# Performance work log

Measured on AMD Instinct MI355X. Metric: run time of the kernel, lower is better.

The kernel has to match this reference:

```python
import jax, jax.numpy as jnp
import numpy as np
from jax import lax


def setup_inputs() -> dict:
    key = jax.random.key(0)
    ks = jax.random.split(key, 8)
    B, H, W = 1, 128, 128

    def rnd(k, shape, fan_in):
        return jax.random.normal(k, shape, dtype=jnp.float32) / np.float32(np.sqrt(fan_in))

    return {
        "x": jax.random.normal(ks[0], (B, 1, H, W), dtype=jnp.float32),
        "z": jax.random.uniform(ks[1], (B, 1), dtype=jnp.float32),
        "w_conv1": rnd(ks[2], (16, 1, 9, 9), 81),
        "b_conv1": jnp.zeros((16,), jnp.float32),
        "w_conv2": rnd(ks[3], (16, 16, 5, 5), 16 * 25),
        "b_conv2": jnp.zeros((16,), jnp.float32),
        "w_fc1": rnd(ks[4], (1024, 128), 1024),
        "b_fc1": jnp.zeros((128,), jnp.float32),
        "w_pose": rnd(ks[5], (1, 16), 1),
        "b_pose": jnp.zeros((16,), jnp.float32),
        "w_fc2": rnd(ks[6], (144, 1), 144),
        "b_fc2": jnp.zeros((1,), jnp.float32),
    }


_DN = ("NCHW", "OIHW", "NCHW")  # conv dimension numbers
_P = 32  # GQ-CNN patch size


def _maxpool2(h):
    return lax.reduce_window(h, -jnp.inf, lax.max, (1, 1, 2, 2), (1, 1, 2, 2), "VALID")


def _gqcnn(patches, z_rep, w_conv1, b_conv1, w_conv2, b_conv2,
           w_fc1, b_fc1, w_pose, b_pose, w_fc2, b_fc2):
    # patches: [N,1,32,32], z_rep: [N,1] -> quality [N,1]
    h = jax.nn.relu(lax.conv_general_dilated(patches, w_conv1, (1, 1), "SAME",
                                             dimension_numbers=_DN)
                    + b_conv1[None, :, None, None])
    h = _maxpool2(h)  # [N,16,16,16]
    h = jax.nn.relu(lax.conv_general_dilated(h, w_conv2, (1, 1), "SAME",
                                             dimension_numbers=_DN)
                    + b_conv2[None, :, None, None])
    h = _maxpool2(h)  # [N,16,8,8]
    flat = h.reshape(h.shape[0], -1)  # [N,1024]
    f = jax.nn.relu(flat @ w_fc1 + b_fc1)      # [N,128]
    p = jax.nn.relu(z_rep @ w_pose + b_pose)   # [N,16]
    return jnp.concatenate([f, p], axis=1) @ w_fc2 + b_fc2  # [N,1]


def reference(x, z, w_conv1, b_conv1, w_conv2, b_conv2,
              w_fc1, b_fc1, w_pose, b_pose, w_fc2, b_fc2):
    B, _, H, W = x.shape
    Hp, Wp = H - _P, W - _P  # loop ranges in the original: range(H-32), range(W-32)
    # Batched patch extraction replaces the O(H*W) Python loop.
    pat = lax.conv_general_dilated_patches(x, (_P, _P), (1, 1), "VALID")  # [B,1024,H-31,W-31]
    pat = pat[:, :, :Hp, :Wp]
    pat = jnp.transpose(pat, (0, 2, 3, 1)).reshape(B * Hp * Wp, 1, _P, _P)
    z_rep = jnp.repeat(z, Hp * Wp, axis=0)  # matches [B,Hp,Wp] flattening order
    q = _gqcnn(pat, z_rep, w_conv1, b_conv1, w_conv2, b_conv2,
               w_fc1, b_fc1, w_pose, b_pose, w_fc2, b_fc2)  # [N,1]
    half = _P // 2
    heat = jnp.zeros_like(x).at[:, :, half:H - half, half:W - half].set(
        q.reshape(B, 1, Hp, Wp))
    return heat
```

## Files before the change

### kernel.cpp

```cpp
#include <hip/hip_runtime.h>

typedef __attribute__((ext_vector_type(8))) short short8;
typedef __attribute__((ext_vector_type(4))) float f32x4;
typedef unsigned short u16;

__device__ __forceinline__ u16 f2bf(float f) {
    unsigned u = __builtin_bit_cast(unsigned, f);
    unsigned r = u + 0x7fffu + ((u >> 16) & 1u);
    return (u16)(r >> 16);
}
__device__ __forceinline__ unsigned pkbf(float lo, float hi) {
    unsigned r;
    asm("v_cvt_pk_bf16_f32 %0, %1, %2" : "=v"(r) : "v"(lo), "v"(hi));
    return r;
}

__global__ __launch_bounds__(256) void k0_prep(
    const float* __restrict__ z, const float* __restrict__ w1,
    const float* __restrict__ w2, const float* __restrict__ wfc1,
    const float* __restrict__ wpose, const float* __restrict__ bpose,
    const float* __restrict__ wfc2, const float* __restrict__ bfc2,
    float* __restrict__ out, u16* __restrict__ w1p, u16* __restrict__ w2p,
    u16* __restrict__ fc1T, float* __restrict__ cst)
{
    int gt = blockIdx.x * 256 + threadIdx.x;
    out[gt] = 0.f;

    if (gt < 2560) {
        int l = (gt >> 3) & 63, j = gt & 7, s = gt >> 9;
        int o = l & 15, bq = l >> 4;
        u16 v = 0;
        if (bq < 3) {
            int dx = bq * 4 + (j & 3);
            int dy = -1;
            if (s < 4) dy = 2 * s + (j >> 2);
            else if (j < 4) dy = 8;
            if (dy >= 0 && dx <= 8) v = f2bf(w1[o * 81 + dy * 9 + dx]);
        }
        w1p[gt] = v;
    }
    if (gt < 6656) {
        int l = (gt >> 3) & 63, j = gt & 7, s = gt >> 9;
        int o = l & 15, bq = l >> 4;
        int dy, dx, c8; bool valid = true;
        if (s < 5)       { dy = s;     dx = bq >> 1;       c8 = bq & 1; }
        else if (s < 10) { dy = s - 5; dx = 2 + (bq >> 1); c8 = bq & 1; }
        else { dy = (s - 10) + 3 * (bq & 1); dx = 4; c8 = bq >> 1; valid = (dy <= 4); }
        int ci = c8 * 8 + j;
        w2p[gt] = valid ? f2bf(w2[o * 400 + ci * 25 + dy * 5 + dx]) : (u16)0;
    }
    {
        int base = gt * 8;
        int n = base >> 10, kk = base & 1023;
        short8 v;
        #pragma unroll
        for (int j = 0; j < 8; ++j) v[j] = (short)f2bf(wfc1[(kk + j) * 128 + n]);
        *(short8*)&fc1T[base] = v;
    }
    if (gt == 0) {
        float zz = z[0];
        float s = bfc2[0];
        for (int j = 0; j < 16; ++j) {
            float p = fmaxf(zz * wpose[j] + bpose[j], 0.f);
            s += p * wfc2[128 + j];
        }
        *cst = s;
    }
}

__global__ __launch_bounds__(256, 2) void k1_feat(
    const float* __restrict__ x, const u16* __restrict__ w1p,
    const u16* __restrict__ w2p, const float* __restrict__ b1g,
    const float* __restrict__ b2g, u16* __restrict__ feat)
{
    __shared__ unsigned s2[40 * 44];
    __shared__ u16 s_h1p[20 * 20 * 24];
    __shared__ unsigned s_feat[512];

    const int tid = threadIdx.x;
    const int lane = tid & 63;
    const int wv = tid >> 6;
    const int mm = lane & 15;
    const int bq = lane >> 4;
    const int blk = blockIdx.x;
    const int py = blk / 96, px = blk % 96;

    {
        uint4 z4 = {0, 0, 0, 0};
        for (int i = tid; i < 152; i += 256) {
            int dst;
            if (i < 88) { int r8 = i / 11, c4 = i % 11;
                          int row = (r8 < 4) ? r8 : 32 + r8; dst = row * 11 + c4; }
            else        { int j = i - 88; dst = (4 + (j >> 1)) * 11 + 9 + (j & 1); }
            ((uint4*)s2)[dst] = z4;
        }
        for (int i = tid; i < 1200; i += 256) ((uint4*)s_h1p)[i] = z4;
    }

    short8 w1f[5], w2f[13];
    #pragma unroll
    for (int s = 0; s < 5; ++s) w1f[s] = *(const short8*)&w1p[(s * 64 + lane) * 8];
    #pragma unroll
    for (int s = 0; s < 13; ++s) w2f[s] = *(const short8*)&w2p[(s * 64 + lane) * 8];
    const float bias1 = b1g[mm], bias2 = b2g[mm];

    for (int task = tid; task < 288; task += 256) {
        int ir = task / 9, g = task - ir * 9;
        int ic0 = g * 4 - 4;
        const float* xr = x + (py + ir) * 128 + px;
        float v[5];
        #pragma unroll
        for (int vi = 0; vi < 5; ++vi) {
            int ic = ic0 + vi;
            v[vi] = (ic >= 0 && ic < 32) ? xr[ic] : 0.f;
        }
        uint4 w;
        w.x = pkbf(v[0], v[1]);
        w.y = pkbf(v[1], v[2]);
        w.z = pkbf(v[2], v[3]);
        w.w = pkbf(v[3], v[4]);
        *(uint4*)&s2[(4 + ir) * 44 + g * 4] = w;
    }
    __syncthreads();

    union F { short8 s; unsigned u[4]; };
    const int dxq = (bq == 3) ? 0 : bq;

    for (int qi = 0; qi < 4; ++qi) {
        int q = wv + qi * 4;
        const unsigned* pb0 = &s2[(2 * q) * 44 + mm + dxq * 4];
        const unsigned* pb1 = pb0 + 16;
        f32x4 ac0 = {0, 0, 0, 0}, ac1 = {0, 0, 0, 0};
        f32x4 ac2 = {0, 0, 0, 0}, ac3 = {0, 0, 0, 0};
        #pragma unroll
        for (int s = 0; s < 5; ++s) {
            const int ra  = 2 * s * 44;
            const int blo = (s < 4) ? (2 * s + 1) * 44 : 9 * 44;
            const int bhi = (s < 4) ? (2 * s + 2) * 44 : 8 * 44;
            F fa0, fa1, fb0, fb1;
            fa0.u[0] = pb0[ra];      fa0.u[1] = pb0[ra + 2];
            fa0.u[2] = pb0[ra + 44]; fa0.u[3] = pb0[ra + 46];
            fa1.u[0] = pb1[ra];      fa1.u[1] = pb1[ra + 2];
            fa1.u[2] = pb1[ra + 44]; fa1.u[3] = pb1[ra + 46];
            fb0.u[0] = pb0[blo];     fb0.u[1] = pb0[blo + 2];
            fb0.u[2] = pb0[bhi];     fb0.u[3] = pb0[bhi + 2];
            fb1.u[0] = pb1[blo];     fb1.u[1] = pb1[blo + 2];
            fb1.u[2] = pb1[bhi];     fb1.u[3] = pb1[bhi + 2];
            ac0 = __builtin_amdgcn_mfma_f32_16x16x32_bf16(fa0.s, w1f[s], ac0, 0, 0, 0);
            ac2 = __builtin_amdgcn_mfma_f32_16x16x32_bf16(fa1.s, w1f[s], ac2, 0, 0, 0);
            ac1 = __builtin_amdgcn_mfma_f32_16x16x32_bf16(fb0.s, w1f[s], ac1, 0, 0, 0);
            ac3 = __builtin_amdgcn_mfma_f32_16x16x32_bf16(fb1.s, w1f[s], ac3, 0, 0, 0);
        }
        #pragma unroll
        for (int h = 0; h < 2; ++h) {
            f32x4 aA = h ? ac2 : ac0, aB = h ? ac3 : ac1;
            float vr0, vr1;
            {
                float a0 = fmaxf(fmaxf(aA[0], aA[1]), fmaxf(aB[0], aB[1]));
                vr0 = fmaxf(a0 + bias1, 0.f);
                float a1 = fmaxf(fmaxf(aA[2], aA[3]), fmaxf(aB[2], aB[3]));
                vr1 = fmaxf(a1 + bias1, 0.f);
            }
            unsigned pw = pkbf(vr0, vr1);
            int pc = h * 8 + (bq << 1);
            int cb = ((2 + q) * 20 + (2 + pc)) * 24 + mm;
            s_h1p[cb] = (u16)pw;
            s_h1p[cb + 24] = (u16)(pw >> 16);
        }
    }
    __syncthreads();

    {
        const int q0 = wv, q1 = wv + 4;
        const int c8s = (bq & 1) * 8;
        const int baseA0 = ((2 * q0) * 20 + mm + (bq >> 1)) * 24 + c8s;
        const int baseA1 = ((2 * q1) * 20 + mm + (bq >> 1)) * 24 + c8s;
        const int baseB0 = baseA0 + 2 * 24;
        const int baseB1 = baseA1 + 2 * 24;
        const int c8C = (bq >> 1) * 8;
        const int yC0 = 2 * q0 + 3 * (bq & 1);
        const int yC1 = 2 * q1 + 3 * (bq & 1);
        f32x4 p0A = {0, 0, 0, 0}, p0B = {0, 0, 0, 0};
        f32x4 p1A = {0, 0, 0, 0}, p1B = {0, 0, 0, 0};

        short8 a0 = *(const short8*)&s_h1p[baseA0];
        short8 a1 = *(const short8*)&s_h1p[baseA1];
        #pragma unroll
        for (int s = 0; s < 5; ++s) {
            short8 n0 = *(const short8*)&s_h1p[baseA0 + (s + 1) * 480];
            short8 n1 = *(const short8*)&s_h1p[baseA1 + (s + 1) * 480];
            p0A = __builtin_amdgcn_mfma_f32_16x16x32_bf16(a0, w2f[s], p0A, 0, 0, 0);
            p1A = __builtin_amdgcn_mfma_f32_16x16x32_bf16(a1, w2f[s], p1A, 0, 0, 0);
            p0B = __builtin_amdgcn_mfma_f32_16x16x32_bf16(n0, w2f[s], p0B, 0, 0, 0);
            p1B = __builtin_amdgcn_mfma_f32_16x16x32_bf16(n1, w2f[s], p1B, 0, 0, 0);
            a0 = n0; a1 = n1;
        }
        a0 = *(const short8*)&s_h1p[baseB0];
        a1 = *(const short8*)&s_h1p[baseB1];
        #pragma unroll
        for (int s = 0; s < 5; ++s) {
            short8 n0 = *(const short8*)&s_h1p[baseB0 + (s + 1) * 480];
            short8 n1 = *(const short8*)&s_h1p[baseB1 + (s + 1) * 480];
            p0A = __builtin_amdgcn_mfma_f32_16x16x32_bf16(a0, w2f[5 + s], p0A, 0, 0, 0);
            p1A = __builtin_amdgcn_mfma_f32_16x16x32_bf16(a1, w2f[5 + s], p1A, 0, 0, 0);
            p0B = __builtin_amdgcn_mfma_f32_16x16x32_bf16(n0, w2f[5 + s], p0B, 0, 0, 0);
            p1B = __builtin_amdgcn_mfma_f32_16x16x32_bf16(n1, w2f[5 + s], p1B, 0, 0, 0);
            a0 = n0; a1 = n1;
        }
        {
            int y00 = yC0, y10 = (yC1 > 19) ? 19 : yC1;
            a0 = *(const short8*)&s_h1p[(y00 * 20 + mm + 4) * 24 + c8C];
            a1 = *(const short8*)&s_h1p[(y10 * 20 + mm + 4) * 24 + c8C];
        }
        #pragma unroll
        for (int s = 0; s < 3; ++s) {
            int y0n = yC0 + s + 1; if (y0n > 19) y0n = 19;
            int y1n = yC1 + s + 1; if (y1n > 19) y1n = 19;
            short8 n0 = *(const short8*)&s_h1p[(y0n * 20 + mm + 4) * 24 + c8C];
            short8 n1 = *(const short8*)&s_h1p[(y1n * 20 + mm + 4) * 24 + c8C];
            p0A = __builtin_amdgcn_mfma_f32_16x16x32_bf16(a0, w2f[10 + s], p0A, 0, 0, 0);
            p1A = __builtin_amdgcn_mfma_f32_16x16x32_bf16(a1, w2f[10 + s], p1A, 0, 0, 0);
            p0B = __builtin_amdgcn_mfma_f32_16x16x32_bf16(n0, w2f[10 + s], p0B, 0, 0, 0);
            p1B = __builtin_amdgcn_mfma_f32_16x16x32_bf16(n1, w2f[10 + s], p1B, 0, 0, 0);
            a0 = n0; a1 = n1;
        }
        #pragma unroll
        for (int pi = 0; pi < 2; ++pi) {
            f32x4 aA = pi ? p1A : p0A, aB = pi ? p1B : p0B;
            int q = pi ? q1 : q0;
            float v0, v1;
            {
                float a = fmaxf(fmaxf(aA[0], aA[1]), fmaxf(aB[0], aB[1]));
                v0 = fmaxf(a + bias2, 0.f);
                float b = fmaxf(fmaxf(aA[2], aA[3]), fmaxf(aB[2], aB[3]));
                v1 = fmaxf(b + bias2, 0.f);
            }
            unsigned dwv = pkbf(v0, v1);
            s_feat[mm * 32 + ((q * 4 + bq) ^ mm)] = dwv;
        }
    }
    __syncthreads();

    {
        int ci = tid >> 4, t = tid & 15;
        uint2 v;
        v.x = s_feat[ci * 32 + ((2 * t) ^ ci)];
        v.y = s_feat[ci * 32 + ((2 * t + 1) ^ ci)];
        *(uint2*)&feat[blk * 1024 + tid * 4] = v;
    }
}

__global__ __launch_bounds__(256) void k2_fc(
    const u16* __restrict__ feat, const u16* __restrict__ fc1T,
    const float* __restrict__ bfc1, const float* __restrict__ wfc2,
    const float* __restrict__ cst, float* __restrict__ out)
{
    __shared__ u16 sA[64 * 136];
    __shared__ u16 sB[128 * 136];
    const int tid = threadIdx.x;
    const int lane = tid & 63;
    const int wv = tid >> 6;
    const int mm = lane & 15;
    const int bq = lane >> 4;
    const int p0 = blockIdx.x * 64;

    f32x4 acc[8];
    #pragma unroll
    for (int i = 0; i < 8; ++i) acc[i] = (f32x4){0, 0, 0, 0};

    for (int kt = 0; kt < 8; ++kt) {
        for (int i = tid; i < 1024; i += 256) {
            int row = i >> 4, ch = i & 15;
            *(short8*)&sA[row * 136 + ch * 8] =
                *(const short8*)&feat[(p0 + row) * 1024 + kt * 128 + ch * 8];
        }
        for (int i = tid; i < 2048; i += 256) {
            int row = i >> 4, ch = i & 15;
            *(short8*)&sB[row * 136 + ch * 8] =
                *(const short8*)&fc1T[row * 1024 + kt * 128 + ch * 8];
        }
        __syncthreads();
        #pragma unroll
        for (int ks = 0; ks < 4; ++ks) {
            short8 aF = *(const short8*)&sA[(wv * 16 + mm) * 136 + ks * 32 + bq * 8];
            #pragma unroll
            for (int nt = 0; nt < 8; ++nt) {
                short8 bF = *(const short8*)&sB[(nt * 16 + mm) * 136 + ks * 32 + bq * 8];
                acc[nt] = __builtin_amdgcn_mfma_f32_16x16x32_bf16(aF, bF, acc[nt], 0, 0, 0);
            }
        }
        __syncthreads();
    }

    const float cpose = *cst;
    float qs[4] = {0, 0, 0, 0};
    #pragma unroll
    for (int nt = 0; nt < 8; ++nt) {
        int n = nt * 16 + mm;
        float bb = bfc1[n], wf = wfc2[n];
        #pragma unroll
        for (int r = 0; r < 4; ++r) {
            float f = fmaxf(acc[nt][r] + bb, 0.f);
            qs[r] += f * wf;
        }
    }
    #pragma unroll
    for (int r = 0; r < 4; ++r) {
        float v = qs[r];
        v += __shfl_xor(v, 1);
        v += __shfl_xor(v, 2);
        v += __shfl_xor(v, 4);
        v += __shfl_xor(v, 8);
        qs[r] = v;
    }
    if (mm == 0) {
        #pragma unroll
        for (int r = 0; r < 4; ++r) {
            int p = p0 + wv * 16 + bq * 4 + r;
            int qy = p / 96, qx = p % 96;
            out[(16 + qy) * 128 + (16 + qx)] = qs[r] + cpose;
        }
    }
}

extern "C" void kernel_launch(void* const* d_in, const int* in_sizes, int n_in,
                              void* d_out, int out_size, void* d_ws, size_t ws_size,
                              hipStream_t stream)
{
    const float* x     = (const float*)d_in[0];
    const float* z     = (const float*)d_in[1];
    const float* w1    = (const float*)d_in[2];
    const float* b1    = (const float*)d_in[3];
    const float* w2    = (const float*)d_in[4];
    const float* b2    = (const float*)d_in[5];
    const float* wfc1  = (const float*)d_in[6];
    const float* bfc1  = (const float*)d_in[7];
    const float* wpose = (const float*)d_in[8];
    const float* bpose = (const float*)d_in[9];
    const float* wfc2  = (const float*)d_in[10];
    const float* bfc2  = (const float*)d_in[11];
    float* out = (float*)d_out;

    char* ws = (char*)d_ws;
    u16*   w1p  = (u16*)(ws + 0);
    u16*   w2p  = (u16*)(ws + 8192);
    float* cst  = (float*)(ws + 22528);
    u16*   fc1T = (u16*)(ws + 24576);
    u16*   feat = (u16*)(ws + 294912);

    hipLaunchKernelGGL(k0_prep, dim3(64), dim3(256), 0, stream,
                       z, w1, w2, wfc1, wpose, bpose, wfc2, bfc2,
                       out, w1p, w2p, fc1T, cst);
    hipLaunchKernelGGL(k1_feat, dim3(9216), dim3(256), 0, stream,
                       x, w1p, w2p, b1, b2, feat);
    hipLaunchKernelGGL(k2_fc, dim3(144), dim3(256), 0, stream,
                       feat, fc1T, bfc1, wfc2, cst, out);
}
```

Measured before the change: 107.6 us.

## Repack conv1 MFMA K-dim, split FC over N with atomics, prefill pose constant

Conv1 weights are repacked so the 9x9 filter fits in 3 MFMA K-steps instead of 5, with a matching change to the shared-memory fragment gathers (the input tile grows two rows). The FC kernel is split across 4 N-slices (576 blocks instead of 144), so each block stages a smaller B tile and combines partial qualities through atomicAdd. The pose/bias constant is now written into the interior of the output in the prep kernel, which removes the separate workspace scalar. This trades fewer MFMAs in the dominant conv kernel and more FC parallelism for atomic traffic and fp32 summation-order nondeterminism.

```diff
diff --git a/kernel.cpp b/kernel.cpp
--- a/kernel.cpp
+++ b/kernel.cpp
@@ -21,22 +21,37 @@
     const float* __restrict__ wpose, const float* __restrict__ bpose,
     const float* __restrict__ wfc2, const float* __restrict__ bfc2,
     float* __restrict__ out, u16* __restrict__ w1p, u16* __restrict__ w2p,
-    u16* __restrict__ fc1T, float* __restrict__ cst)
+    u16* __restrict__ fc1T)
 {
     int gt = blockIdx.x * 256 + threadIdx.x;
-    out[gt] = 0.f;
-
-    if (gt < 2560) {
+
+    {
+        float zz = z[0];
+        float s = bfc2[0];
+        #pragma unroll
+        for (int j = 0; j < 16; ++j) {
+            float p = fmaxf(zz * wpose[j] + bpose[j], 0.f);
+            s += p * wfc2[128 + j];
+        }
+        int y = gt >> 7, x = gt & 127;
+        bool interior = (y >= 16) && (y < 112) && (x >= 16) && (x < 112);
+        out[gt] = interior ? s : 0.f;
+    }
+
+    if (gt < 1536) {
         int l = (gt >> 3) & 63, j = gt & 7, s = gt >> 9;
         int o = l & 15, bq = l >> 4;
+        int dy = -1, dx = -1;
+        if (s < 2) { dy = s * 4 + bq; dx = j; }
+        else {
+            int p = j >> 1, hi = j & 1;
+            if (bq == 0)      { dy = 8;         dx = j; }
+            else if (bq == 1) { dy = 2 * p;     dx = 8 + hi; }
+            else if (bq == 2) { dy = 2 * p + 1; dx = 8 + hi; }
+            else              { dy = (j == 0) ? 8 : -1; dx = 8; }
+        }
         u16 v = 0;
-        if (bq < 3) {
-            int dx = bq * 4 + (j & 3);
-            int dy = -1;
-            if (s < 4) dy = 2 * s + (j >> 2);
-            else if (j < 4) dy = 8;
-            if (dy >= 0 && dx <= 8) v = f2bf(w1[o * 81 + dy * 9 + dx]);
-        }
+        if (dy >= 0 && dy < 9 && dx >= 0 && dx < 9) v = f2bf(w1[o * 81 + dy * 9 + dx]);
         w1p[gt] = v;
     }
     if (gt < 6656) {
@@ -57,15 +72,6 @@
         for (int j = 0; j < 8; ++j) v[j] = (short)f2bf(wfc1[(kk + j) * 128 + n]);
         *(short8*)&fc1T[base] = v;
     }
-    if (gt == 0) {
-        float zz = z[0];
-        float s = bfc2[0];
-        for (int j = 0; j < 16; ++j) {
-            float p = fmaxf(zz * wpose[j] + bpose[j], 0.f);
-            s += p * wfc2[128 + j];
-        }
-        *cst = s;
-    }
 }
 
 __global__ __launch_bounds__(256, 2) void k1_feat(
@@ -73,7 +79,7 @@
     const u16* __restrict__ w2p, const float* __restrict__ b1g,
     const float* __restrict__ b2g, u16* __restrict__ feat)
 {
-    __shared__ unsigned s2[40 * 44];
+    __shared__ unsigned s2[42 * 44];
     __shared__ u16 s_h1p[20 * 20 * 24];
     __shared__ unsigned s_feat[512];
 
@@ -87,19 +93,19 @@
 
     {
         uint4 z4 = {0, 0, 0, 0};
-        for (int i = tid; i < 152; i += 256) {
+        for (int i = tid; i < 174; i += 256) {
             int dst;
-            if (i < 88) { int r8 = i / 11, c4 = i % 11;
-                          int row = (r8 < 4) ? r8 : 32 + r8; dst = row * 11 + c4; }
-            else        { int j = i - 88; dst = (4 + (j >> 1)) * 11 + 9 + (j & 1); }
+            if (i < 110) { int r10 = i / 11, c4 = i % 11;
+                           int row = (r10 < 4) ? r10 : 32 + r10; dst = row * 11 + c4; }
+            else         { int j = i - 110; dst = (4 + (j >> 1)) * 11 + 9 + (j & 1); }
             ((uint4*)s2)[dst] = z4;
         }
         for (int i = tid; i < 1200; i += 256) ((uint4*)s_h1p)[i] = z4;
     }
 
-    short8 w1f[5], w2f[13];
+    short8 w1f[3], w2f[13];
     #pragma unroll
-    for (int s = 0; s < 5; ++s) w1f[s] = *(const short8*)&w1p[(s * 64 + lane) * 8];
+    for (int s = 0; s < 3; ++s) w1f[s] = *(const short8*)&w1p[(s * 64 + lane) * 8];
     #pragma unroll
     for (int s = 0; s < 13; ++s) w2f[s] = *(const short8*)&w2p[(s * 64 + lane) * 8];
     const float bias1 = b1g[mm], bias2 = b2g[mm];
@@ -124,32 +130,50 @@
     __syncthreads();
 
     union F { short8 s; unsigned u[4]; };
-    const int dxq = (bq == 3) ? 0 : bq;
+    const int bq44 = bq * 44;
+    int k2b, k2s;
+    if (bq == 0)      { k2b = 352; k2s = 2; }
+    else if (bq == 1) { k2b = 8;   k2s = 88; }
+    else if (bq == 2) { k2b = 52;  k2s = 88; }
+    else              { k2b = 360; k2s = 2; }
 
     for (int qi = 0; qi < 4; ++qi) {
         int q = wv + qi * 4;
-        const unsigned* pb0 = &s2[(2 * q) * 44 + mm + dxq * 4];
-        const unsigned* pb1 = pb0 + 16;
+        const unsigned* pb = &s2[(2 * q) * 44 + mm];
+        const unsigned* pq = pb + bq44;
         f32x4 ac0 = {0, 0, 0, 0}, ac1 = {0, 0, 0, 0};
         f32x4 ac2 = {0, 0, 0, 0}, ac3 = {0, 0, 0, 0};
         #pragma unroll
-        for (int s = 0; s < 5; ++s) {
-            const int ra  = 2 * s * 44;
-            const int blo = (s < 4) ? (2 * s + 1) * 44 : 9 * 44;
-            const int bhi = (s < 4) ? (2 * s + 2) * 44 : 8 * 44;
-            F fa0, fa1, fb0, fb1;
-            fa0.u[0] = pb0[ra];      fa0.u[1] = pb0[ra + 2];
-            fa0.u[2] = pb0[ra + 44]; fa0.u[3] = pb0[ra + 46];
-            fa1.u[0] = pb1[ra];      fa1.u[1] = pb1[ra + 2];
-            fa1.u[2] = pb1[ra + 44]; fa1.u[3] = pb1[ra + 46];
-            fb0.u[0] = pb0[blo];     fb0.u[1] = pb0[blo + 2];
-            fb0.u[2] = pb0[bhi];     fb0.u[3] = pb0[bhi + 2];
-            fb1.u[0] = pb1[blo];     fb1.u[1] = pb1[blo + 2];
-            fb1.u[2] = pb1[bhi];     fb1.u[3] = pb1[bhi + 2];
+        for (int s = 0; s < 2; ++s) {
+            const int o0 = s * 176;
+            F fa0, fb0, fa1, fb1;
+            fa0.u[0] = pq[o0];      fa0.u[1] = pq[o0 + 2];
+            fa0.u[2] = pq[o0 + 4];  fa0.u[3] = pq[o0 + 6];
+            fa1.u[0] = pq[o0 + 16]; fa1.u[1] = pq[o0 + 18];
+            fa1.u[2] = pq[o0 + 20]; fa1.u[3] = pq[o0 + 22];
+            fb0.u[0] = pq[o0 + 44]; fb0.u[1] = pq[o0 + 46];
+            fb0.u[2] = pq[o0 + 48]; fb0.u[3] = pq[o0 + 50];
+            fb1.u[0] = pq[o0 + 60]; fb1.u[1] = pq[o0 + 62];
+            fb1.u[2] = pq[o0 + 64]; fb1.u[3] = pq[o0 + 66];
             ac0 = __builtin_amdgcn_mfma_f32_16x16x32_bf16(fa0.s, w1f[s], ac0, 0, 0, 0);
             ac2 = __builtin_amdgcn_mfma_f32_16x16x32_bf16(fa1.s, w1f[s], ac2, 0, 0, 0);
             ac1 = __builtin_amdgcn_mfma_f32_16x16x32_bf16(fb0.s, w1f[s], ac1, 0, 0, 0);
             ac3 = __builtin_amdgcn_mfma_f32_16x16x32_bf16(fb1.s, w1f[s], ac3, 0, 0, 0);
+        }
+        {
+            F fa0, fb0, fa1, fb1;
+            #pragma unroll
+            for (int p = 0; p < 4; ++p) {
+                int o = k2b + p * k2s;
+                fa0.u[p] = pb[o];
+                fb0.u[p] = pb[o + 44];
+                fa1.u[p] = pb[o + 16];
+                fb1.u[p] = pb[o + 60];
+            }
+            ac0 = __builtin_amdgcn_mfma_f32_16x16x32_bf16(fa0.s, w1f[2], ac0, 0, 0, 0);
+            ac2 = __builtin_amdgcn_mfma_f32_16x16x32_bf16(fa1.s, w1f[2], ac2, 0, 0, 0);
+            ac1 = __builtin_amdgcn_mfma_f32_16x16x32_bf16(fb0.s, w1f[2], ac1, 0, 0, 0);
+            ac3 = __builtin_amdgcn_mfma_f32_16x16x32_bf16(fb1.s, w1f[2], ac3, 0, 0, 0);
         }
         #pragma unroll
         for (int h = 0; h < 2; ++h) {
@@ -253,20 +277,21 @@
 __global__ __launch_bounds__(256) void k2_fc(
     const u16* __restrict__ feat, const u16* __restrict__ fc1T,
     const float* __restrict__ bfc1, const float* __restrict__ wfc2,
-    const float* __restrict__ cst, float* __restrict__ out)
+    float* __restrict__ out)
 {
     __shared__ u16 sA[64 * 136];
-    __shared__ u16 sB[128 * 136];
+    __shared__ u16 sB[32 * 136];
     const int tid = threadIdx.x;
     const int lane = tid & 63;
     const int wv = tid >> 6;
     const int mm = lane & 15;
     const int bq = lane >> 4;
-    const int p0 = blockIdx.x * 64;
-
-    f32x4 acc[8];
-    #pragma unroll
-    for (int i = 0; i < 8; ++i) acc[i] = (f32x4){0, 0, 0, 0};
+    const int p0 = (blockIdx.x % 144) * 64;
+    const int n0 = (blockIdx.x / 144) * 32;
+
+    f32x4 acc[2];
+    acc[0] = (f32x4){0, 0, 0, 0};
+    acc[1] = (f32x4){0, 0, 0, 0};
 
     for (int kt = 0; kt < 8; ++kt) {
         for (int i = tid; i < 1024; i += 256) {
@@ -274,17 +299,17 @@
             *(short8*)&sA[row * 136 + ch * 8] =
                 *(const short8*)&feat[(p0 + row) * 1024 + kt * 128 + ch * 8];
         }
-        for (int i = tid; i < 2048; i += 256) {
+        for (int i = tid; i < 512; i += 256) {
             int row = i >> 4, ch = i & 15;
             *(short8*)&sB[row * 136 + ch * 8] =
-                *(const short8*)&fc1T[row * 1024 + kt * 128 + ch * 8];
+                *(const short8*)&fc1T[(n0 + row) * 1024 + kt * 128 + ch * 8];
         }
         __syncthreads();
         #pragma unroll
         for (int ks = 0; ks < 4; ++ks) {
             short8 aF = *(const short8*)&sA[(wv * 16 + mm) * 136 + ks * 32 + bq * 8];
             #pragma unroll
-            for (int nt = 0; nt < 8; ++nt) {
+            for (int nt = 0; nt < 2; ++nt) {
                 short8 bF = *(const short8*)&sB[(nt * 16 + mm) * 136 + ks * 32 + bq * 8];
                 acc[nt] = __builtin_amdgcn_mfma_f32_16x16x32_bf16(aF, bF, acc[nt], 0, 0, 0);
             }
@@ -292,11 +317,10 @@
         __syncthreads();
     }
 
-    const float cpose = *cst;
     float qs[4] = {0, 0, 0, 0};
     #pragma unroll
-    for (int nt = 0; nt < 8; ++nt) {
-        int n = nt * 16 + mm;
+    for (int nt = 0; nt < 2; ++nt) {
+        int n = n0 + nt * 16 + mm;
         float bb = bfc1[n], wf = wfc2[n];
         #pragma unroll
         for (int r = 0; r < 4; ++r) {
@@ -318,7 +342,7 @@
         for (int r = 0; r < 4; ++r) {
             int p = p0 + wv * 16 + bq * 4 + r;
             int qy = p / 96, qx = p % 96;
-            out[(16 + qy) * 128 + (16 + qx)] = qs[r] + cpose;
+            atomicAdd(&out[(16 + qy) * 128 + (16 + qx)], qs[r]);
         }
     }
 }
@@ -343,16 +367,15 @@
 
     char* ws = (char*)d_ws;
     u16*   w1p  = (u16*)(ws + 0);
-    u16*   w2p  = (u16*)(ws + 8192);
-    float* cst  = (float*)(ws + 22528);
+    u16*   w2p  = (u16*)(ws + 4096);
     u16*   fc1T = (u16*)(ws + 24576);
     u16*   feat = (u16*)(ws + 294912);
 
     hipLaunchKernelGGL(k0_prep, dim3(64), dim3(256), 0, stream,
                        z, w1, w2, wfc1, wpose, bpose, wfc2, bfc2,
-                       out, w1p, w2p, fc1T, cst);
+                       out, w1p, w2p, fc1T);
     hipLaunchKernelGGL(k1_feat, dim3(9216), dim3(256), 0, stream,
                        x, w1p, w2p, b1, b2, feat);
-    hipLaunchKernelGGL(k2_fc, dim3(144), dim3(256), 0, stream,
-                       feat, fc1T, bfc1, wfc2, cst, out);
-}
+    hipLaunchKernelGGL(k2_fc, dim3(576), dim3(256), 0, stream,
+                       feat, fc1T, bfc1, wfc2, out);
+}
```

Measured after the change: 113.1 us. +5.1%, slower.
